# Performance work log

Hardware: AMD Instinct MI355X
Metric: run time of the kernel (lower is better)

Reference implementation:

```python
import jax, jax.numpy as jnp
import numpy as np

N_NODES = 100000
N_EDGES = 1600000
DIM = 64
NEG_SLOPE = 0.2  # DGL GATConv default
BN_EPS = 1e-5


def setup_inputs() -> dict:
    key = jax.random.key(0)
    ks = jax.random.split(key, 16)
    d = {}
    d["node_weight"] = jax.random.normal(ks[0], (N_NODES, DIM), jnp.float32)
    d["edge_weight"] = jax.random.normal(ks[1], (N_EDGES,), jnp.float32)  # unused in forward (faithful to source)
    d["src"] = jax.random.randint(ks[2], (N_EDGES,), 0, N_NODES)
    d["dst"] = jax.random.randint(ks[3], (N_EDGES,), 0, N_NODES)
    i = 4
    scale = 1.0 / np.sqrt(DIM)
    for l in (1, 2, 3):
        d[f"W{l}"] = jax.random.normal(ks[i], (DIM, DIM), jnp.float32) * scale; i += 1
        d[f"al{l}"] = jax.random.normal(ks[i], (DIM,), jnp.float32) * 0.1; i += 1
        d[f"ar{l}"] = jax.random.normal(ks[i], (DIM,), jnp.float32) * 0.1; i += 1
        d[f"b{l}"] = jnp.zeros((DIM,), jnp.float32)
        d[f"g{l}"] = jnp.ones((DIM,), jnp.float32)
        d[f"beta{l}"] = jnp.zeros((DIM,), jnp.float32)
    return d


def gat_layer(h, src, dst, W, al, ar, b):
    # DGL GATConv, 1 head: project, edge attention, per-dst softmax, scatter-add
    feat = h @ W                                  # [N, D]
    el = feat @ al                                # [N]
    er = feat @ ar                                # [N]
    e = jax.nn.leaky_relu(el[src] + er[dst], NEG_SLOPE)   # [E]
    m = jax.ops.segment_max(e, dst, num_segments=N_NODES)  # per-dst max
    ex = jnp.exp(e - m[dst])
    s = jax.ops.segment_sum(ex, dst, num_segments=N_NODES)
    alpha = ex / s[dst]                           # edge softmax
    out = jax.ops.segment_sum(alpha[:, None] * feat[src], dst, num_segments=N_NODES)
    return out + b


def batchnorm(h, g, beta):
    # BatchNorm1d in training mode: batch stats, biased variance
    mu = jnp.mean(h, axis=0)
    var = jnp.mean(jnp.square(h - mu), axis=0)
    return (h - mu) * jax.lax.rsqrt(var + BN_EPS) * g + beta


def reference(node_weight, edge_weight, src, dst,
              W1, al1, ar1, b1, g1, beta1,
              W2, al2, ar2, b2, g2, beta2,
              W3, al3, ar3, b3, g3, beta3):
    # dropout is identity in eval mode
    h = gat_layer(node_weight, src, dst, W1, al1, ar1, b1)
    h = jax.nn.elu(batchnorm(h, g1, beta1))
    h = gat_layer(h, src, dst, W2, al2, ar2, b2)
    h = jax.nn.elu(batchnorm(h, g2, beta2))
    h = gat_layer(h, src, dst, W3, al3, ar3, b3)
    h = batchnorm(h, g3, beta3)
    return h
```

## Files before the change

kernel.cpp:

```cpp
#include <hip/hip_runtime.h>
#include <hip/hip_bf16.h>
#include <math.h>

#define DIM 64
#define BSHIFT 9
#define BNODES 512
#define MAXB 256
#define EPT 8
#define CHUNK 2048

typedef __attribute__((ext_vector_type(8))) short bf16x8;
typedef __attribute__((ext_vector_type(4))) float f32x4;

__device__ __forceinline__ short f2bf(float x) {
    union { __hip_bfloat16 b; short s; } u;
    u.b = __float2bfloat16(x);
    return u.s;
}
__device__ __forceinline__ float bf2f(short s) {
    return __uint_as_float(((unsigned)(unsigned short)s) << 16);
}


__global__ void bin_count_kernel(const int* __restrict__ dst, int* __restrict__ bucket_cnt, int E) {
    __shared__ int h[MAXB];
    int t = threadIdx.x;
    h[t] = 0;
    __syncthreads();
    for (int i = blockIdx.x * blockDim.x + t; i < E; i += gridDim.x * blockDim.x)
        atomicAdd(&h[dst[i] >> BSHIFT], 1);
    __syncthreads();
    if (h[t]) atomicAdd(&bucket_cnt[t], h[t]);
}

__global__ void bucket_scan_kernel(const int* __restrict__ bucket_cnt,
                                   int* __restrict__ bucket_off, int* __restrict__ bucket_fill) {
    __shared__ int s[MAXB];
    int t = threadIdx.x;
    int v = bucket_cnt[t];
    s[t] = v;
    __syncthreads();
    for (int off = 1; off < MAXB; off <<= 1) {
        int x = (t >= off) ? s[t - off] : 0;
        __syncthreads();
        s[t] += x;
        __syncthreads();
    }
    bucket_off[t] = s[t] - v;
    bucket_fill[t] = 0;
}

__global__ __launch_bounds__(256) void bin_scatter_kernel(
    const int* __restrict__ src, const int* __restrict__ dst,
    const int* __restrict__ bucket_off, int* __restrict__ bucket_fill,
    unsigned long long* __restrict__ binned, int E) {
    __shared__ int lcnt[MAXB];
    __shared__ int lbase[MAXB];
    int t = threadIdx.x;
    lcnt[t] = 0;
    __syncthreads();
    int base = blockIdx.x * CHUNK;
    unsigned long long pair[EPT];
    int slot[EPT];
#pragma unroll
    for (int j = 0; j < EPT; j++) {
        int idx = base + j * 256 + t;
        if (idx < E) {
            int s = src[idx], d = dst[idx];
            pair[j] = ((unsigned long long)(unsigned)d << 32) | (unsigned)s;
            slot[j] = atomicAdd(&lcnt[d >> BSHIFT], 1);
        } else {
            slot[j] = -1;
        }
    }
    __syncthreads();
    int c = lcnt[t];
    if (c) lbase[t] = atomicAdd(&bucket_fill[t], c);
    __syncthreads();
#pragma unroll
    for (int j = 0; j < EPT; j++) {
        if (slot[j] >= 0) {
            int b = (int)(pair[j] >> 32) >> BSHIFT;
            binned[(size_t)bucket_off[b] + lbase[b] + slot[j]] = pair[j];
        }
    }
}

__global__ __launch_bounds__(256) void csr_finalize_kernel(
    const unsigned long long* __restrict__ binned, const int* __restrict__ bucket_off,
    const int* __restrict__ bucket_cnt, int* __restrict__ row_ptr,
    int* __restrict__ src_sorted, int N, int E, int nbuck) {
    __shared__ int cnt[BNODES];
    __shared__ int excl[BNODES];
    __shared__ int ps[256];
    int b = blockIdx.x, t = threadIdx.x;
    for (int i = t; i < BNODES; i += 256) cnt[i] = 0;
    __syncthreads();
    int s0 = bucket_off[b], c = bucket_cnt[b];
    for (int i = t; i < c; i += 256)
        atomicAdd(&cnt[(int)(binned[(size_t)s0 + i] >> 32) & (BNODES - 1)], 1);
    __syncthreads();
    int a0 = cnt[2 * t], a1 = cnt[2 * t + 1];
    int pairsum = a0 + a1;
    ps[t] = pairsum;
    __syncthreads();
    for (int off = 1; off < 256; off <<= 1) {
        int x = (t >= off) ? ps[t - off] : 0;
        __syncthreads();
        ps[t] += x;
        __syncthreads();
    }
    int run = ps[t] - pairsum;
    excl[2 * t] = run;
    excl[2 * t + 1] = run + a0;
    __syncthreads();
    int nbase = b << BSHIFT;
    for (int i = t; i < BNODES; i += 256)
        if (nbase + i < N) row_ptr[nbase + i] = s0 + excl[i];
    if (b == nbuck - 1 && t == 0) row_ptr[N] = E;
    for (int i = t; i < BNODES; i += 256) cnt[i] = 0;
    __syncthreads();
    for (int i = t; i < c; i += 256) {
        unsigned long long p = binned[(size_t)s0 + i];
        int d = (int)(p >> 32) & (BNODES - 1);
        int pos = excl[d] + atomicAdd(&cnt[d], 1);
        src_sorted[(size_t)s0 + pos] = (int)(p & 0xffffffffu);
    }
}


__global__ void wlr_kernel(
    const float* __restrict__ W1, const float* __restrict__ al1, const float* __restrict__ ar1,
    const float* __restrict__ W2, const float* __restrict__ al2, const float* __restrict__ ar2,
    const float* __restrict__ W3, const float* __restrict__ al3, const float* __restrict__ ar3,
    float* __restrict__ wlr, short* __restrict__ wfrag,
    int* __restrict__ bucket_cnt, float* __restrict__ stats) {
    const float* W  = (blockIdx.x == 0) ? W1  : (blockIdx.x == 1) ? W2  : W3;
    const float* al = (blockIdx.x == 0) ? al1 : (blockIdx.x == 1) ? al2 : al3;
    const float* ar = (blockIdx.x == 0) ? ar1 : (blockIdx.x == 1) ? ar2 : ar3;
    int t = threadIdx.x;
    if (blockIdx.x == 0) bucket_cnt[t] = 0;
    if (blockIdx.x == 1) { stats[t] = 0.f; if (t < 128) stats[256 + t] = 0.f; }
    short* whi = wfrag + blockIdx.x * 8192;
    short* wlo = whi + 4096;
    for (int idx = t; idx < 4096; idx += 256) {
        int j = idx & 7, li = (idx >> 3) & 15, quad = (idx >> 7) & 3;
        int nt = (idx >> 9) & 3, ks = idx >> 11;
        int k = ks * 32 + quad * 8 + j, nn = nt * 16 + li;
        float w = W[k * 64 + nn];
        short hi = f2bf(w);
        whi[idx] = hi;
        wlo[idx] = f2bf(w - bf2f(hi));
    }
    if (t < 64) {
        float l = 0.f, r = 0.f;
        for (int nn = 0; nn < 64; nn++) {
            float w = W[t * 64 + nn];
            l = fmaf(w, al[nn], l);
            r = fmaf(w, ar[nn], r);
        }
        const float LOG2E = 1.4426950408889634f;
        wlr[blockIdx.x * 128 + t] = l * LOG2E;
        wlr[blockIdx.x * 128 + 64 + t] = r * LOG2E;
    }
}

__global__ __launch_bounds__(256) void gemm64_mfma_kernel(
    const void* __restrict__ hvoid, int in_bf16, const short* __restrict__ wfrag_l,
    const float* __restrict__ wl, const float* __restrict__ wr,
    const float* __restrict__ stats, const float* __restrict__ g,
    const float* __restrict__ beta, int do_bn, float invN,
    __hip_bfloat16* __restrict__ feat, float* __restrict__ el, float* __restrict__ er,
    int n) {
    int t = threadIdx.x;
    int lane = t & 63;
    int li = lane & 15;
    int quad = lane >> 4;
    int wv = t >> 6;

    const short* whi = wfrag_l;
    const short* wlo = wfrag_l + 4096;
    bf16x8 b_hi[2][4], b_lo[2][4];
#pragma unroll
    for (int ks = 0; ks < 2; ks++)
#pragma unroll
        for (int nt = 0; nt < 4; nt++) {
            int base = (((ks * 4 + nt) * 4 + quad) * 16 + li) * 8;
            b_hi[ks][nt] = *(const bf16x8*)(whi + base);
            b_lo[ks][nt] = *(const bf16x8*)(wlo + base);
        }
    float wlv[2][8], wrv[2][8];
#pragma unroll
    for (int ks = 0; ks < 2; ks++)
#pragma unroll
        for (int j = 0; j < 8; j++) {
            wlv[ks][j] = wl[ks * 32 + quad * 8 + j];
            wrv[ks][j] = wr[ks * 32 + quad * 8 + j];
        }

    float sc[2][8], sh[2][8];
    if (do_bn) {
#pragma unroll
        for (int ks = 0; ks < 2; ks++)
#pragma unroll
            for (int j = 0; j < 8; j++) {
                int k = ks * 32 + quad * 8 + j;
                float mu = stats[k] * invN;
                float var = fmaf(-mu, mu, stats[64 + k] * invN);
                float inv = rsqrtf(var + 1e-5f) * g[k];
                sc[ks][j] = inv;
                sh[ks][j] = beta[k] - mu * inv;
            }
    }

    int ntiles = (n + 15) >> 4;
    for (int tile = blockIdx.x * 4 + wv; tile < ntiles; tile += gridDim.x * 4) {
        int m0 = tile << 4;
        int rrow = m0 + li;
        size_t rowbase = (size_t)((rrow < n) ? rrow : (n - 1)) * 64;
        bf16x8 a_hi[2], a_lo[2];
        float elp = 0.f, erp = 0.f;
#pragma unroll
        for (int ks = 0; ks < 2; ks++) {
            float x[8];
            if (in_bf16) {
                const unsigned short* rp = (const unsigned short*)hvoid + rowbase + ks * 32 + quad * 8;
                uint4 pv = *(const uint4*)rp;
                x[0] = bf2f((short)(pv.x & 0xffffu)); x[1] = bf2f((short)(pv.x >> 16));
                x[2] = bf2f((short)(pv.y & 0xffffu)); x[3] = bf2f((short)(pv.y >> 16));
                x[4] = bf2f((short)(pv.z & 0xffffu)); x[5] = bf2f((short)(pv.z >> 16));
                x[6] = bf2f((short)(pv.w & 0xffffu)); x[7] = bf2f((short)(pv.w >> 16));
            } else {
                const float* rp = (const float*)hvoid + rowbase + ks * 32 + quad * 8;
                float4 v0 = *(const float4*)rp;
                float4 v1 = *(const float4*)(rp + 4);
                x[0] = v0.x; x[1] = v0.y; x[2] = v0.z; x[3] = v0.w;
                x[4] = v1.x; x[5] = v1.y; x[6] = v1.z; x[7] = v1.w;
            }
#pragma unroll
            for (int j = 0; j < 8; j++) {
                float v = x[j];
                if (do_bn) {
                    v = fmaf(v, sc[ks][j], sh[ks][j]);
                    if (v < 0.f) v = expm1f(v);
                }
                elp = fmaf(v, wlv[ks][j], elp);
                erp = fmaf(v, wrv[ks][j], erp);
                short hi = f2bf(v);
                a_hi[ks][j] = hi;
                a_lo[ks][j] = f2bf(v - bf2f(hi));
            }
        }
        elp += __shfl_xor(elp, 16, 64);
        elp += __shfl_xor(elp, 32, 64);
        erp += __shfl_xor(erp, 16, 64);
        erp += __shfl_xor(erp, 32, 64);
        if (lane < 16 && m0 + li < n) {
            el[m0 + li] = elp;
            er[m0 + li] = erp;
        }
        f32x4 acc[4];
#pragma unroll
        for (int nt = 0; nt < 4; nt++) acc[nt] = (f32x4){0.f, 0.f, 0.f, 0.f};
#pragma unroll
        for (int ks = 0; ks < 2; ks++)
#pragma unroll
            for (int nt = 0; nt < 4; nt++) {
                acc[nt] = __builtin_amdgcn_mfma_f32_16x16x32_bf16(a_hi[ks], b_hi[ks][nt], acc[nt], 0, 0, 0);
                acc[nt] = __builtin_amdgcn_mfma_f32_16x16x32_bf16(a_lo[ks], b_hi[ks][nt], acc[nt], 0, 0, 0);
                acc[nt] = __builtin_amdgcn_mfma_f32_16x16x32_bf16(a_hi[ks], b_lo[ks][nt], acc[nt], 0, 0, 0);
            }
#pragma unroll
        for (int nt = 0; nt < 4; nt++)
#pragma unroll
            for (int reg = 0; reg < 4; reg++) {
                int wrow = m0 + quad * 4 + reg;
                if (wrow < n) {
                    union { __hip_bfloat16 b; short s; } u;
                    u.s = f2bf(acc[nt][reg]);
                    feat[(size_t)wrow * 64 + nt * 16 + li] = u.b;
                }
            }
    }
}

#define AGG_LOAD(P, ELV, POS)                                  \
    {                                                          \
        int idx = (POS) + q;                                   \
        bool v = idx < end;                                    \
        int idc = v ? idx : end - 1;                           \
        int sn = src_sorted[idc];                              \
        float ev = el[sn];                                     \
        ELV = v ? ev : -INFINITY;                              \
        P = featv[(size_t)sn * 8 + li];                        \
    }

#define AGG_CHUNK(P, ELV)                                      \
    {                                                          \
        float e = ELV + er_n;                                  \
        e = fmaxf(e, 0.2f * e);                                \
        float w = exp2f(e);                                    \
        s += w;                                                \
        a0 = fmaf(w, __uint_as_float(P.x << 16), a0);          \
        a1 = fmaf(w, __uint_as_float(P.x & 0xffff0000u), a1);  \
        a2 = fmaf(w, __uint_as_float(P.y << 16), a2);          \
        a3 = fmaf(w, __uint_as_float(P.y & 0xffff0000u), a3);  \
        a4 = fmaf(w, __uint_as_float(P.z << 16), a4);          \
        a5 = fmaf(w, __uint_as_float(P.z & 0xffff0000u), a5);  \
        a6 = fmaf(w, __uint_as_float(P.w << 16), a6);          \
        a7 = fmaf(w, __uint_as_float(P.w & 0xffff0000u), a7);  \
    }

__global__ __launch_bounds__(256) void attn_agg_kernel(
    const int* __restrict__ row_ptr, const int* __restrict__ src_sorted,
    const float* __restrict__ el, const float* __restrict__ er,
    const __hip_bfloat16* __restrict__ feat, const float* __restrict__ bias,
    void* __restrict__ outv, int out_bf16, int n) {
    int t = threadIdx.x, lane = t & 63;
    int q = lane >> 3;
    int li = lane & 7;
    int d = li * 8 + ((q & 1) << 2) + (q & 2) + ((q >> 2) & 1);
    float bias_d = bias[d];
    const uint4* featv = (const uint4*)feat;

    for (int base = blockIdx.x * 16; base < n; base += gridDim.x * 16) {
        int node0 = base + (t >> 6) * 4;
#pragma unroll
        for (int j = 0; j < 4; j++) {
            int node = node0 + j;
            if (node >= n) break;
            int start = row_ptr[node], end = row_ptr[node + 1];
            float er_n = er[node];

            float s = 0.f;
            float a0 = 0.f, a1 = 0.f, a2 = 0.f, a3 = 0.f;
            float a4 = 0.f, a5 = 0.f, a6 = 0.f, a7 = 0.f;

            uint4 pA = {0u, 0u, 0u, 0u}, pB = {0u, 0u, 0u, 0u};
            float elA = -INFINITY, elB = -INFINITY;
            if (start < end) AGG_LOAD(pA, elA, start)
            if (start + 8 < end) AGG_LOAD(pB, elB, start + 8)
            for (int i = start; i < end; i += 16) {
                AGG_CHUNK(pA, elA)
                if (i + 16 < end) AGG_LOAD(pA, elA, i + 16)
                if (i + 8 < end) {
                    AGG_CHUNK(pB, elB)
                    if (i + 24 < end) AGG_LOAD(pB, elB, i + 24)
                }
            }
            s += __shfl_xor(s, 8, 64);
            s += __shfl_xor(s, 16, 64);
            s += __shfl_xor(s, 32, 64);
            bool b0 = (q & 1) != 0;
            float t0 = __shfl_xor(a0, 8, 64), t1 = __shfl_xor(a1, 8, 64);
            float t2 = __shfl_xor(a2, 8, 64), t3 = __shfl_xor(a3, 8, 64);
            float t4 = __shfl_xor(a4, 8, 64), t5 = __shfl_xor(a5, 8, 64);
            float t6 = __shfl_xor(a6, 8, 64), t7 = __shfl_xor(a7, 8, 64);
            float x0 = b0 ? (a4 + t4) : (a0 + t0);
            float x1 = b0 ? (a5 + t5) : (a1 + t1);
            float y0 = b0 ? (a6 + t6) : (a2 + t2);
            float y1 = b0 ? (a7 + t7) : (a3 + t3);
            bool b1 = (q & 2) != 0;
            float u0 = __shfl_xor(x0, 16, 64), u1 = __shfl_xor(x1, 16, 64);
            float v0 = __shfl_xor(y0, 16, 64), v1 = __shfl_xor(y1, 16, 64);
            float z0 = b1 ? (y0 + v0) : (x0 + u0);
            float z1 = b1 ? (y1 + v1) : (x1 + u1);
            z0 += __shfl_xor(z0, 32, 64);
            z1 += __shfl_xor(z1, 32, 64);
            float val = ((q & 4) != 0) ? z1 : z0;
            float inv_s = (s > 0.f) ? 1.f / s : 0.f;
            float x = fmaf(val, inv_s, bias_d);
            if (out_bf16) {
                union { __hip_bfloat16 b; short s2; } u;
                u.s2 = f2bf(x);
                ((__hip_bfloat16*)outv)[(size_t)node * 64 + d] = u.b;
            } else {
                ((float*)outv)[(size_t)node * 64 + d] = x;
            }
        }
    }
}

__global__ __launch_bounds__(256) void bn_stats_kernel(const void* __restrict__ hvoid,
                                                       int in_bf16,
                                                       float* __restrict__ stats, int n) {
    __shared__ float ls[256], lss[256];
    int t = threadIdx.x, lane = t & 63;
    int w = blockIdx.x * 4 + (t >> 6);
    int stride = gridDim.x * 4;
    float s = 0.f, ss = 0.f;
    for (int row = w; row < n; row += stride) {
        float v;
        if (in_bf16) v = bf2f((short)((const unsigned short*)hvoid)[(size_t)row * DIM + lane]);
        else         v = ((const float*)hvoid)[(size_t)row * DIM + lane];
        s += v;
        ss = fmaf(v, v, ss);
    }
    ls[t] = s; lss[t] = ss;
    __syncthreads();
    if (t < 64) {
        float a = ls[t] + ls[t + 64] + ls[t + 128] + ls[t + 192];
        float b = lss[t] + lss[t + 64] + lss[t + 128] + lss[t + 192];
        atomicAdd(&stats[t], a);
        atomicAdd(&stats[64 + t], b);
    }
}

__global__ void bn_apply_kernel(float* __restrict__ h, const float* __restrict__ stats,
                                const float* __restrict__ g, const float* __restrict__ beta,
                                int n, int do_elu) {
    int i = blockIdx.x * blockDim.x + threadIdx.x;
    int total = n * DIM;
    int stride = gridDim.x * blockDim.x;
    float invN = 1.f / (float)n;
    for (; i < total; i += stride) {
        int c = i & 63;
        float mu = stats[c] * invN;
        float var = fmaf(-mu, mu, stats[DIM + c] * invN);
        float x = (h[i] - mu) * rsqrtf(var + 1e-5f) * g[c] + beta[c];
        if (do_elu && x < 0.f) x = expm1f(x);
        h[i] = x;
    }
}


extern "C" void kernel_launch(void* const* d_in, const int* in_sizes, int n_in,
                              void* d_out, int out_size, void* d_ws, size_t ws_size,
                              hipStream_t stream) {
    const float* nw = (const float*)d_in[0];
    const int* src = (const int*)d_in[2];
    const int* dst = (const int*)d_in[3];
    const int N = in_sizes[0] / DIM;
    const int E = in_sizes[2];
    const float invN = 1.f / (float)N;
    const int nbuck = (N + BNODES - 1) >> BSHIFT;

    char* ws = (char*)d_ws;
    size_t off = 0;
    auto alloc = [&](size_t bytes) -> void* {
        void* p = ws + off;
        off += (bytes + 255) & ~(size_t)255;
        return p;
    };
    int* row_ptr      = (int*)alloc(((size_t)N + 1) * 4);
    int* bucket_cnt   = (int*)alloc(MAXB * 4);
    int* bucket_off   = (int*)alloc(MAXB * 4);
    int* bucket_fill  = (int*)alloc(MAXB * 4);
    unsigned long long* binned = (unsigned long long*)alloc((size_t)E * 8);
    int* src_sorted   = (int*)alloc((size_t)E * 4);
    float* el         = (float*)alloc((size_t)N * 4);
    float* er         = (float*)alloc((size_t)N * 4);
    __hip_bfloat16* feat = (__hip_bfloat16*)alloc((size_t)N * DIM * 2);
    __hip_bfloat16* hbuf = (__hip_bfloat16*)alloc((size_t)N * DIM * 2);
    float* stats      = (float*)alloc(3 * 512);
    float* wlr        = (float*)alloc(3 * 128 * 4);
    short* wfrag      = (short*)alloc(3 * 8192 * 2);

    int ntiles = (N + 15) >> 4;
    int attn_grid = (N + 15) / 16;
    if (attn_grid > 2048) attn_grid = 2048;

    wlr_kernel<<<3, 256, 0, stream>>>(
        (const float*)d_in[4],  (const float*)d_in[5],  (const float*)d_in[6],
        (const float*)d_in[10], (const float*)d_in[11], (const float*)d_in[12],
        (const float*)d_in[16], (const float*)d_in[17], (const float*)d_in[18],
        wlr, wfrag, bucket_cnt, stats);
    bin_count_kernel<<<256, 256, 0, stream>>>(dst, bucket_cnt, E);
    bucket_scan_kernel<<<1, MAXB, 0, stream>>>(bucket_cnt, bucket_off, bucket_fill);
    bin_scatter_kernel<<<(E + CHUNK - 1) / CHUNK, 256, 0, stream>>>(
        src, dst, bucket_off, bucket_fill, binned, E);
    csr_finalize_kernel<<<nbuck, 256, 0, stream>>>(binned, bucket_off, bucket_cnt,
                                                   row_ptr, src_sorted, N, E, nbuck);

    for (int l = 0; l < 3; l++) {
        const float* b    = (const float*)d_in[7 + 6 * l];
        const void* hin   = (l == 0) ? (const void*)nw : (const void*)hbuf;
        int in_bf16       = (l == 0) ? 0 : 1;
        void* hout        = (l == 2) ? (void*)d_out : (void*)hbuf;
        int out_bf16      = (l == 2) ? 0 : 1;
        float* stats_prev = (l == 0) ? stats : stats + (l - 1) * 128;
        float* stats_cur  = stats + l * 128;

        gemm64_mfma_kernel<<<(ntiles + 15) / 16, 256, 0, stream>>>(
            hin, in_bf16, wfrag + l * 8192,
            wlr + l * 128, wlr + l * 128 + 64,
            stats_prev,
            (l == 0) ? (const float*)d_in[8] : (const float*)d_in[8 + 6 * (l - 1)],
            (l == 0) ? (const float*)d_in[9] : (const float*)d_in[9 + 6 * (l - 1)],
            (l > 0) ? 1 : 0, invN,
            feat, el, er, N);
        attn_agg_kernel<<<attn_grid, 256, 0, stream>>>(row_ptr, src_sorted, el, er,
                                                       feat, b, hout, out_bf16, N);
        bn_stats_kernel<<<512, 256, 0, stream>>>(hout, out_bf16, stats_cur, N);
    }
    bn_apply_kernel<<<2048, 256, 0, stream>>>((float*)d_out, stats + 2 * 128,
                                              (const float*)d_in[8 + 12],
                                              (const float*)d_in[9 + 12],
                                              N, 0);
}
```

Measured before the change: 446.3 us.

## Merge histogram into prep kernel and vectorize batchnorm stats and apply

Folds the destination-bucket histogram into the weight-prep kernel as extra blocks that write per-block histograms, which the scan kernel then reduces. This removes one kernel launch and the global atomics on bucket counts. It also vectorizes the batchnorm stats kernel (each thread reads 8 channels per row with 16-byte loads) and the apply kernel (float4 per thread). The cost is a 256x256 histogram buffer in workspace and a serial 256-iteration reduction in the single-block scan.

```diff
diff --git a/kernel.cpp b/kernel.cpp
--- a/kernel.cpp
+++ b/kernel.cpp
@@ -22,124 +22,27 @@
 }
 
 
-__global__ void bin_count_kernel(const int* __restrict__ dst, int* __restrict__ bucket_cnt, int E) {
-    __shared__ int h[MAXB];
-    int t = threadIdx.x;
-    h[t] = 0;
-    __syncthreads();
-    for (int i = blockIdx.x * blockDim.x + t; i < E; i += gridDim.x * blockDim.x)
-        atomicAdd(&h[dst[i] >> BSHIFT], 1);
-    __syncthreads();
-    if (h[t]) atomicAdd(&bucket_cnt[t], h[t]);
-}
-
-__global__ void bucket_scan_kernel(const int* __restrict__ bucket_cnt,
-                                   int* __restrict__ bucket_off, int* __restrict__ bucket_fill) {
-    __shared__ int s[MAXB];
-    int t = threadIdx.x;
-    int v = bucket_cnt[t];
-    s[t] = v;
-    __syncthreads();
-    for (int off = 1; off < MAXB; off <<= 1) {
-        int x = (t >= off) ? s[t - off] : 0;
-        __syncthreads();
-        s[t] += x;
-        __syncthreads();
-    }
-    bucket_off[t] = s[t] - v;
-    bucket_fill[t] = 0;
-}
-
-__global__ __launch_bounds__(256) void bin_scatter_kernel(
-    const int* __restrict__ src, const int* __restrict__ dst,
-    const int* __restrict__ bucket_off, int* __restrict__ bucket_fill,
-    unsigned long long* __restrict__ binned, int E) {
-    __shared__ int lcnt[MAXB];
-    __shared__ int lbase[MAXB];
-    int t = threadIdx.x;
-    lcnt[t] = 0;
-    __syncthreads();
-    int base = blockIdx.x * CHUNK;
-    unsigned long long pair[EPT];
-    int slot[EPT];
-#pragma unroll
-    for (int j = 0; j < EPT; j++) {
-        int idx = base + j * 256 + t;
-        if (idx < E) {
-            int s = src[idx], d = dst[idx];
-            pair[j] = ((unsigned long long)(unsigned)d << 32) | (unsigned)s;
-            slot[j] = atomicAdd(&lcnt[d >> BSHIFT], 1);
-        } else {
-            slot[j] = -1;
-        }
-    }
-    __syncthreads();
-    int c = lcnt[t];
-    if (c) lbase[t] = atomicAdd(&bucket_fill[t], c);
-    __syncthreads();
-#pragma unroll
-    for (int j = 0; j < EPT; j++) {
-        if (slot[j] >= 0) {
-            int b = (int)(pair[j] >> 32) >> BSHIFT;
-            binned[(size_t)bucket_off[b] + lbase[b] + slot[j]] = pair[j];
-        }
-    }
-}
-
-__global__ __launch_bounds__(256) void csr_finalize_kernel(
-    const unsigned long long* __restrict__ binned, const int* __restrict__ bucket_off,
-    const int* __restrict__ bucket_cnt, int* __restrict__ row_ptr,
-    int* __restrict__ src_sorted, int N, int E, int nbuck) {
-    __shared__ int cnt[BNODES];
-    __shared__ int excl[BNODES];
-    __shared__ int ps[256];
-    int b = blockIdx.x, t = threadIdx.x;
-    for (int i = t; i < BNODES; i += 256) cnt[i] = 0;
-    __syncthreads();
-    int s0 = bucket_off[b], c = bucket_cnt[b];
-    for (int i = t; i < c; i += 256)
-        atomicAdd(&cnt[(int)(binned[(size_t)s0 + i] >> 32) & (BNODES - 1)], 1);
-    __syncthreads();
-    int a0 = cnt[2 * t], a1 = cnt[2 * t + 1];
-    int pairsum = a0 + a1;
-    ps[t] = pairsum;
-    __syncthreads();
-    for (int off = 1; off < 256; off <<= 1) {
-        int x = (t >= off) ? ps[t - off] : 0;
-        __syncthreads();
-        ps[t] += x;
-        __syncthreads();
-    }
-    int run = ps[t] - pairsum;
-    excl[2 * t] = run;
-    excl[2 * t + 1] = run + a0;
-    __syncthreads();
-    int nbase = b << BSHIFT;
-    for (int i = t; i < BNODES; i += 256)
-        if (nbase + i < N) row_ptr[nbase + i] = s0 + excl[i];
-    if (b == nbuck - 1 && t == 0) row_ptr[N] = E;
-    for (int i = t; i < BNODES; i += 256) cnt[i] = 0;
-    __syncthreads();
-    for (int i = t; i < c; i += 256) {
-        unsigned long long p = binned[(size_t)s0 + i];
-        int d = (int)(p >> 32) & (BNODES - 1);
-        int pos = excl[d] + atomicAdd(&cnt[d], 1);
-        src_sorted[(size_t)s0 + pos] = (int)(p & 0xffffffffu);
-    }
-}
-
-
-__global__ void wlr_kernel(
+__global__ __launch_bounds__(256) void prep_kernel(
     const float* __restrict__ W1, const float* __restrict__ al1, const float* __restrict__ ar1,
     const float* __restrict__ W2, const float* __restrict__ al2, const float* __restrict__ ar2,
     const float* __restrict__ W3, const float* __restrict__ al3, const float* __restrict__ ar3,
-    float* __restrict__ wlr, short* __restrict__ wfrag,
-    int* __restrict__ bucket_cnt, float* __restrict__ stats) {
+    float* __restrict__ wlr, short* __restrict__ wfrag, float* __restrict__ stats,
+    const int* __restrict__ dst, int* __restrict__ hist, int E) {
+    int t = threadIdx.x;
+    if (blockIdx.x >= 3) {
+        __shared__ int h[MAXB];
+        int cb = blockIdx.x - 3;
+        h[t] = 0;
+        __syncthreads();
+        for (int i = cb * 256 + t; i < E; i += 256 * 256)
+            atomicAdd(&h[dst[i] >> BSHIFT], 1);
+        __syncthreads();
+        hist[cb * MAXB + t] = h[t];
+        return;
+    }
     const float* W  = (blockIdx.x == 0) ? W1  : (blockIdx.x == 1) ? W2  : W3;
     const float* al = (blockIdx.x == 0) ? al1 : (blockIdx.x == 1) ? al2 : al3;
     const float* ar = (blockIdx.x == 0) ? ar1 : (blockIdx.x == 1) ? ar2 : ar3;
-    int t = threadIdx.x;
-    if (blockIdx.x == 0) bucket_cnt[t] = 0;
     if (blockIdx.x == 1) { stats[t] = 0.f; if (t < 128) stats[256 + t] = 0.f; }
     short* whi = wfrag + blockIdx.x * 8192;
     short* wlo = whi + 4096;
@@ -164,6 +67,106 @@
         wlr[blockIdx.x * 128 + 64 + t] = r * LOG2E;
     }
 }
+
+__global__ void bucket_scan_kernel(const int* __restrict__ hist,
+                                   int* __restrict__ bucket_cnt,
+                                   int* __restrict__ bucket_off, int* __restrict__ bucket_fill) {
+    __shared__ int s[MAXB];
+    int t = threadIdx.x;
+    int v = 0;
+#pragma unroll 8
+    for (int b = 0; b < 256; b++) v += hist[b * MAXB + t];
+    bucket_cnt[t] = v;
+    s[t] = v;
+    __syncthreads();
+    for (int off = 1; off < MAXB; off <<= 1) {
+        int x = (t >= off) ? s[t - off] : 0;
+        __syncthreads();
+        s[t] += x;
+        __syncthreads();
+    }
+    bucket_off[t] = s[t] - v;
+    bucket_fill[t] = 0;
+}
+
+__global__ __launch_bounds__(256) void bin_scatter_kernel(
+    const int* __restrict__ src, const int* __restrict__ dst,
+    const int* __restrict__ bucket_off, int* __restrict__ bucket_fill,
+    unsigned long long* __restrict__ binned, int E) {
+    __shared__ int lcnt[MAXB];
+    __shared__ int lbase[MAXB];
+    int t = threadIdx.x;
+    lcnt[t] = 0;
+    __syncthreads();
+    int base = blockIdx.x * CHUNK;
+    unsigned long long pair[EPT];
+    int slot[EPT];
+#pragma unroll
+    for (int j = 0; j < EPT; j++) {
+        int idx = base + j * 256 + t;
+        if (idx < E) {
+            int s = src[idx], d = dst[idx];
+            pair[j] = ((unsigned long long)(unsigned)d << 32) | (unsigned)s;
+            slot[j] = atomicAdd(&lcnt[d >> BSHIFT], 1);
+        } else {
+            slot[j] = -1;
+        }
+    }
+    __syncthreads();
+    int c = lcnt[t];
+    if (c) lbase[t] = atomicAdd(&bucket_fill[t], c);
+    __syncthreads();
+#pragma unroll
+    for (int j = 0; j < EPT; j++) {
+        if (slot[j] >= 0) {
+            int b = (int)(pair[j] >> 32) >> BSHIFT;
+            binned[(size_t)bucket_off[b] + lbase[b] + slot[j]] = pair[j];
+        }
+    }
+}
+
+__global__ __launch_bounds__(256) void csr_finalize_kernel(
+    const unsigned long long* __restrict__ binned, const int* __restrict__ bucket_off,
+    const int* __restrict__ bucket_cnt, int* __restrict__ row_ptr,
+    int* __restrict__ src_sorted, int N, int E, int nbuck) {
+    __shared__ int cnt[BNODES];
+    __shared__ int excl[BNODES];
+    __shared__ int ps[256];
+    int b = blockIdx.x, t = threadIdx.x;
+    for (int i = t; i < BNODES; i += 256) cnt[i] = 0;
+    __syncthreads();
+    int s0 = bucket_off[b], c = bucket_cnt[b];
+    for (int i = t; i < c; i += 256)
+        atomicAdd(&cnt[(int)(binned[(size_t)s0 + i] >> 32) & (BNODES - 1)], 1);
+    __syncthreads();
+    int a0 = cnt[2 * t], a1 = cnt[2 * t + 1];
+    int pairsum = a0 + a1;
+    ps[t] = pairsum;
+    __syncthreads();
+    for (int off = 1; off < 256; off <<= 1) {
+        int x = (t >= off) ? ps[t - off] : 0;
+        __syncthreads();
+        ps[t] += x;
+        __syncthreads();
+    }
+    int run = ps[t] - pairsum;
+    excl[2 * t] = run;
+    excl[2 * t + 1] = run + a0;
+    __syncthreads();
+    int nbase = b << BSHIFT;
+    for (int i = t; i < BNODES; i += 256)
+        if (nbase + i < N) row_ptr[nbase + i] = s0 + excl[i];
+    if (b == nbuck - 1 && t == 0) row_ptr[N] = E;
+    for (int i = t; i < BNODES; i += 256) cnt[i] = 0;
+    __syncthreads();
+    for (int i = t; i < c; i += 256) {
+        unsigned long long p = binned[(size_t)s0 + i];
+        int d = (int)(p >> 32) & (BNODES - 1);
+        int pos = excl[d] + atomicAdd(&cnt[d], 1);
+        src_sorted[(size_t)s0 + pos] = (int)(p & 0xffffffffu);
+    }
+}
+
 
 __global__ __launch_bounds__(256) void gemm64_mfma_kernel(
     const void* __restrict__ hvoid, int in_bf16, const short* __restrict__ wfrag_l,
@@ -384,23 +387,47 @@
 __global__ __launch_bounds__(256) void bn_stats_kernel(const void* __restrict__ hvoid,
                                                        int in_bf16,
                                                        float* __restrict__ stats, int n) {
-    __shared__ float ls[256], lss[256];
-    int t = threadIdx.x, lane = t & 63;
-    int w = blockIdx.x * 4 + (t >> 6);
-    int stride = gridDim.x * 4;
-    float s = 0.f, ss = 0.f;
-    for (int row = w; row < n; row += stride) {
-        float v;
-        if (in_bf16) v = bf2f((short)((const unsigned short*)hvoid)[(size_t)row * DIM + lane]);
-        else         v = ((const float*)hvoid)[(size_t)row * DIM + lane];
-        s += v;
-        ss = fmaf(v, v, ss);
-    }
-    ls[t] = s; lss[t] = ss;
+    __shared__ float lp[256][8];
+    __shared__ float lq[256][8];
+    int t = threadIdx.x;
+    int rs = t >> 3;
+    int oc = t & 7;
+    float s[8], ss[8];
+#pragma unroll
+    for (int j = 0; j < 8; j++) { s[j] = 0.f; ss[j] = 0.f; }
+    for (int row = blockIdx.x * 32 + rs; row < n; row += gridDim.x * 32) {
+        float x[8];
+        if (in_bf16) {
+            const unsigned short* rp = (const unsigned short*)hvoid + (size_t)row * 64 + oc * 8;
+            uint4 pv = *(const uint4*)rp;
+            x[0] = bf2f((short)(pv.x & 0xffffu)); x[1] = bf2f((short)(pv.x >> 16));
+            x[2] = bf2f((short)(pv.y & 0xffffu)); x[3] = bf2f((short)(pv.y >> 16));
+            x[4] = bf2f((short)(pv.z & 0xffffu)); x[5] = bf2f((short)(pv.z >> 16));
+            x[6] = bf2f((short)(pv.w & 0xffffu)); x[7] = bf2f((short)(pv.w >> 16));
+        } else {
+            const float* rp = (const float*)hvoid + (size_t)row * 64 + oc * 8;
+            float4 v0 = *(const float4*)rp;
+            float4 v1 = *(const float4*)(rp + 4);
+            x[0] = v0.x; x[1] = v0.y; x[2] = v0.z; x[3] = v0.w;
+            x[4] = v1.x; x[5] = v1.y; x[6] = v1.z; x[7] = v1.w;
+        }
+#pragma unroll
+        for (int j = 0; j < 8; j++) {
+            s[j] += x[j];
+            ss[j] = fmaf(x[j], x[j], ss[j]);
+        }
+    }
+#pragma unroll
+    for (int j = 0; j < 8; j++) { lp[t][j] = s[j]; lq[t][j] = ss[j]; }
     __syncthreads();
     if (t < 64) {
-        float a = ls[t] + ls[t + 64] + ls[t + 128] + ls[t + 192];
-        float b = lss[t] + lss[t + 64] + lss[t + 128] + lss[t + 192];
+        int o = t >> 3, j = t & 7;
+        float a = 0.f, b = 0.f;
+#pragma unroll 8
+        for (int r2 = 0; r2 < 32; r2++) {
+            a += lp[r2 * 8 + o][j];
+            b += lq[r2 * 8 + o][j];
+        }
         atomicAdd(&stats[t], a);
         atomicAdd(&stats[64 + t], b);
     }
@@ -410,16 +437,24 @@
                                 const float* __restrict__ g, const float* __restrict__ beta,
                                 int n, int do_elu) {
     int i = blockIdx.x * blockDim.x + threadIdx.x;
-    int total = n * DIM;
+    int total4 = n * 16;
     int stride = gridDim.x * blockDim.x;
     float invN = 1.f / (float)n;
-    for (; i < total; i += stride) {
-        int c = i & 63;
-        float mu = stats[c] * invN;
-        float var = fmaf(-mu, mu, stats[DIM + c] * invN);
-        float x = (h[i] - mu) * rsqrtf(var + 1e-5f) * g[c] + beta[c];
-        if (do_elu && x < 0.f) x = expm1f(x);
-        h[i] = x;
+    for (; i < total4; i += stride) {
+        float4 v = ((const float4*)h)[i];
+        int c0 = (i & 15) * 4;
+        float vv[4] = {v.x, v.y, v.z, v.w};
+#pragma unroll
+        for (int k = 0; k < 4; k++) {
+            int c = c0 + k;
+            float mu = stats[c] * invN;
+            float var = fmaf(-mu, mu, stats[64 + c] * invN);
+            float x = (vv[k] - mu) * rsqrtf(var + 1e-5f) * g[c] + beta[c];
+            if (do_elu && x < 0.f) x = expm1f(x);
+            vv[k] = x;
+        }
+        float4 o = {vv[0], vv[1], vv[2], vv[3]};
+        ((float4*)h)[i] = o;
     }
 }
 
@@ -446,6 +481,7 @@
     int* bucket_cnt   = (int*)alloc(MAXB * 4);
     int* bucket_off   = (int*)alloc(MAXB * 4);
     int* bucket_fill  = (int*)alloc(MAXB * 4);
+    int* hist         = (int*)alloc((size_t)MAXB * 256 * 4);
     unsigned long long* binned = (unsigned long long*)alloc((size_t)E * 8);
     int* src_sorted   = (int*)alloc((size_t)E * 4);
     float* el         = (float*)alloc((size_t)N * 4);
@@ -460,13 +496,12 @@
     int attn_grid = (N + 15) / 16;
     if (attn_grid > 2048) attn_grid = 2048;
 
-    wlr_kernel<<<3, 256, 0, stream>>>(
+    prep_kernel<<<3 + 256, 256, 0, stream>>>(
         (const float*)d_in[4],  (const float*)d_in[5],  (const float*)d_in[6],
         (const float*)d_in[10], (const float*)d_in[11], (const float*)d_in[12],
         (const float*)d_in[16], (const float*)d_in[17], (const float*)d_in[18],
-        wlr, wfrag, bucket_cnt, stats);
-    bin_count_kernel<<<256, 256, 0, stream>>>(dst, bucket_cnt, E);
-    bucket_scan_kernel<<<1, MAXB, 0, stream>>>(bucket_cnt, bucket_off, bucket_fill);
+        wlr, wfrag, stats, dst, hist, E);
+    bucket_scan_kernel<<<1, MAXB, 0, stream>>>(hist, bucket_cnt, bucket_off, bucket_fill);
     bin_scatter_kernel<<<(E + CHUNK - 1) / CHUNK, 256, 0, stream>>>(
         src, dst, bucket_off, bucket_fill, binned, E);
     csr_finalize_kernel<<<nbuck, 256, 0, stream>>>(binned, bucket_off, bucket_cnt,
```

After: 436.4 us (median of 2 runs). 2.2% less time.
